# Performance work log

Measured on AMD Instinct MI355X. Metric: run time of the kernel, lower is better.

Reference implementation:

```python
import jax, jax.numpy as jnp
import numpy as np

PRIME_DELAYS = (1, 2, 3, 5)
LOCAL_LR = 0.05  # base_local_lr after clamp to [0, 0.99]


def _apply_delays(x, delay_gains):
    """OCNS phasal delay embedding. x: [B,T,D,2], delay_gains: [n_delays,D,2]."""
    x_eff = x
    for idx, tau in enumerate(PRIME_DELAYS):
        gr = delay_gains[idx, :, 0]
        gi = delay_gains[idx, :, 1]
        dr = x[:, :-tau, :, 0]
        di = x[:, :-tau, :, 1]
        upd = jnp.stack([dr * gr - di * gi, dr * gi + di * gr], axis=-1)
        x_eff = x_eff.at[:, tau:].add(upd)
    return x_eff


def _moe_expert_choice(xf, gate_bias, W_router, W1, W2, capacity):
    """Expert-choice MoE: each expert picks its top-`capacity` tokens.
    xf: [N,F] flattened complex features; returns [N,F]."""
    logits = xf @ W_router + gate_bias              # [N,E]
    scores = jax.nn.softmax(logits, axis=-1)        # [N,E]
    topv, topi = jax.lax.top_k(scores.T, capacity)  # each [E,C]
    xe = xf[topi]                                   # [E,C,F] gather
    h = jax.nn.gelu(jnp.einsum('ecf,efh->ech', xe, W1))
    ye = jnp.einsum('ech,ehf->ecf', h, W2) * topv[..., None]
    N, F = xf.shape
    return jnp.zeros((N, F), xf.dtype).at[topi.reshape(-1)].add(ye.reshape(-1, F))


def _forward(x_stream, delay_gains, Wg_spec, W_router, W1, W2, cos_p, sin_p, local_iters):
    x = jnp.nan_to_num(x_stream.astype(jnp.float32))
    B, T, D, _ = x.shape
    N = B * T
    E = W_router.shape[1]
    capacity = (2 * N) // E  # top-2-equivalent expert-choice token budget

    # spectral gate bias: per-token spectral magnitude -> expert logit bias [N,E]
    mag = jnp.sqrt(x[..., 0] ** 2 + x[..., 1] ** 2 + 1e-8)
    gate_bias = mag.reshape(N, D) @ Wg_spec

    # phase-rotated target: x_target[:, t] = rot(x[:, t-1]); x_target[:, 0] = x[:, 0]
    prev = x[:, :-1]
    rot_r = prev[..., 0] * cos_p - prev[..., 1] * sin_p
    rot_i = prev[..., 0] * sin_p + prev[..., 1] * cos_p
    x_target = jnp.concatenate([x[:, :1], jnp.stack([rot_r, rot_i], axis=-1)], axis=1)

    def step(xc, _):
        x_eff = _apply_delays(xc, delay_gains)
        pred = _moe_expert_choice(x_eff.reshape(N, 2 * D), gate_bias, W_router, W1, W2, capacity)
        pred = pred.reshape(B, T, D, 2)
        upd = jnp.clip(LOCAL_LR * (x_target - pred), -10.0, 10.0)
        return xc + upd, None

    out, _ = jax.lax.scan(step, x, None, length=local_iters)
    return out


def setup_inputs() -> dict:
    key = jax.random.key(0)
    ks = jax.random.split(key, 8)
    B, T, D, E = 2, 2048, 256, 64
    F = 2 * D
    phase = jax.random.uniform(ks[0], (D,)) * 2.0 * np.pi
    return {
        'x_stream': jax.random.normal(ks[1], (B, T, D, 2), jnp.float32) * 0.5,
        'delay_gains': jax.random.normal(ks[2], (len(PRIME_DELAYS), D, 2), jnp.float32) * 0.02,
        'Wg_spec': jax.random.normal(ks[3], (D, E), jnp.float32) / np.sqrt(D),
        'W_router': jax.random.normal(ks[4], (F, E), jnp.float32) / np.sqrt(F),
        'W1': jax.random.normal(ks[5], (E, F, F), jnp.float32) / np.sqrt(F),
        'W2': jax.random.normal(ks[6], (E, F, F), jnp.float32) / np.sqrt(F),
        'cos_p': jnp.cos(phase),
        'sin_p': jnp.sin(phase),
        'local_iters': 8,
    }


def reference(x_stream, delay_gains, Wg_spec, W_router, W1, W2, cos_p, sin_p, local_iters):
    return _forward(x_stream, delay_gains, Wg_spec, W_router, W1, W2, cos_p, sin_p, local_iters)
```

## Files before the change

kernel.cpp:

```cpp
#include <hip/hip_runtime.h>
#include <hip/hip_bf16.h>

#define TB 2
#define TT 2048
#define TD 256
#define TE 64
#define TF 512
#define TN 4096
#define TCAP 128
#define NITER 8

typedef __attribute__((ext_vector_type(8))) short bf16x8;
typedef __attribute__((ext_vector_type(4))) float f32x4;

__device__ inline float sanitize(float v){
  if (v != v) return 0.0f;
  const float FMAX = 3.402823466e+38f;
  if (v >  FMAX) return  FMAX;
  if (v < -FMAX) return -FMAX;
  return v;
}

__device__ inline short f2bf(float f){
  union { __hip_bfloat16 h; short s; } u;
  u.h = __float2bfloat16(f);
  return u.s;
}

__device__ inline float gelu_tanh(float x){
  float x3 = x*x*x;
  return 0.5f*x*(1.0f + tanhf(0.7978845608028654f*(x + 0.044715f*x3)));
}

__device__ __forceinline__ void gload16(const void* g, void* l){
  __builtin_amdgcn_global_load_lds(
      (__attribute__((address_space(1))) void*)g,
      (__attribute__((address_space(3))) void*)l, 16, 0, 0);
}


__global__ void k_init(const float* __restrict__ xs, const float* __restrict__ cosp,
                       const float* __restrict__ sinp, float* __restrict__ xw,
                       float* __restrict__ xt){
  int idx = blockIdx.x*256 + threadIdx.x;
  if (idx >= TN*TD) return;
  int d = idx & (TD-1);
  int n = idx >> 8;
  int t = n & (TT-1);
  float xr = sanitize(xs[2*idx]), xi = sanitize(xs[2*idx+1]);
  xw[2*idx] = xr; xw[2*idx+1] = xi;
  float tr, ti;
  if (t == 0){ tr = xr; ti = xi; }
  else {
    float pr = sanitize(xs[2*(idx-TD)]), pi = sanitize(xs[2*(idx-TD)+1]);
    float c = cosp[d], s = sinp[d];
    tr = pr*c - pi*s;
    ti = pr*s + pi*c;
  }
  xt[2*idx] = tr; xt[2*idx+1] = ti;
}

__global__ __launch_bounds__(64) void k_gatebias(const float* __restrict__ xw,
                                                 const float* __restrict__ wg,
                                                 float* __restrict__ gb){
  __shared__ float mag[TD];
  int n = blockIdx.x, t = threadIdx.x;
  for (int d = t; d < TD; d += 64){
    float xr = xw[(size_t)n*TF + 2*d], xi = xw[(size_t)n*TF + 2*d + 1];
    mag[d] = sqrtf(xr*xr + xi*xi + 1e-8f);
  }
  __syncthreads();
  float acc = 0.f;
  for (int d = 0; d < TD; d++) acc += mag[d]*wg[d*TE + t];
  gb[(size_t)n*TE + t] = acc;
}

__global__ __launch_bounds__(256) void k_castw(const float* __restrict__ W, short* __restrict__ Wt){
  __shared__ float tile[64][68];
  int e = blockIdx.y;
  int kt = (blockIdx.x >> 3) * 64;
  int nt = (blockIdx.x & 7) * 64;
  int tid = threadIdx.x;
  {
    int row = tid >> 4;
    int c4 = (tid & 15) * 4;
    #pragma unroll
    for (int i = 0; i < 4; i++){
      int r = row + i*16;
      float4 v = *(const float4*)(W + ((size_t)e*TF + kt + r)*TF + nt + c4);
      *(float4*)&tile[r][c4] = v;
    }
  }
  __syncthreads();
  #pragma unroll
  for (int i = 0; i < 2; i++){
    int un = tid + i*256;
    int nrow = un >> 3;
    int k8 = (un & 7) * 8;
    bf16x8 o;
    #pragma unroll
    for (int j = 0; j < 8; j++) o[j] = f2bf(tile[k8+j][nrow]);
    *(bf16x8*)(Wt + ((size_t)e*TF + nt + nrow)*TF + kt + k8) = o;
  }
}


__global__ __launch_bounds__(256) void k_combine(
    const float* __restrict__ xOld, float* __restrict__ xNew,
    const float* __restrict__ xt, const float* __restrict__ ye,
    const int* __restrict__ cnt, const int* __restrict__ list)
{
  int tid = threadIdx.x;
  int tok = tid >> 5;
  int kq  = (tid & 31) * 16;
  int n   = blockIdx.x*8 + tok;
  size_t off = (size_t)n*TF + kq;
  float p[16];
  #pragma unroll
  for (int q = 0; q < 16; q++) p[q] = 0.f;
  int c = cnt[n];
  for (int j = 0; j < c; j++){
    const float4* s = (const float4*)(ye + (size_t)list[n*64 + j]*TF + kq);
    #pragma unroll
    for (int k4 = 0; k4 < 4; k4++){
      float4 v = s[k4];
      p[4*k4+0] += v.x; p[4*k4+1] += v.y; p[4*k4+2] += v.z; p[4*k4+3] += v.w;
    }
  }
  const float4* a4 = (const float4*)(xOld + off);
  const float4* t4 = (const float4*)(xt + off);
  float4* o4 = (float4*)(xNew + off);
  #pragma unroll
  for (int j = 0; j < 4; j++){
    float4 a = a4[j], t = t4[j], o;
    float u;
    u = 0.05f*(t.x - p[4*j+0]); u = fminf(10.f, fmaxf(-10.f, u)); o.x = a.x + u;
    u = 0.05f*(t.y - p[4*j+1]); u = fminf(10.f, fmaxf(-10.f, u)); o.y = a.y + u;
    u = 0.05f*(t.z - p[4*j+2]); u = fminf(10.f, fmaxf(-10.f, u)); o.z = a.z + u;
    u = 0.05f*(t.w - p[4*j+3]); u = fminf(10.f, fmaxf(-10.f, u)); o.w = a.w + u;
    o4[j] = o;
  }
}


__global__ __launch_bounds__(256) void k_fuse2(
    const float* __restrict__ xcur, const float* __restrict__ g,
    const float* __restrict__ wr, const float* __restrict__ gb,
    short* __restrict__ xbf, float* __restrict__ scoresT)
{
  __shared__ float xeff[8][516];
  __shared__ float Bt[64][68];
  int tid = threadIdx.x;
  int tok = tid >> 5;
  int lane5 = tid & 31;
  int kq  = lane5 * 16;
  int n   = blockIdx.x*8 + tok;
  int t   = n & (TT-1);
  size_t rowoff = (size_t)n*TF + kq;

  float eff[16];
  {
    const float4* a4 = (const float4*)(xcur + rowoff);
    #pragma unroll
    for (int j = 0; j < 4; j++){
      float4 v = a4[j];
      eff[4*j+0] = v.x; eff[4*j+1] = v.y; eff[4*j+2] = v.z; eff[4*j+3] = v.w;
    }
  }
  const int taus[4] = {1,2,3,5};
  int d0 = kq >> 1;
  #pragma unroll
  for (int i = 0; i < 4; i++){
    int tau = taus[i];
    if (t >= tau){
      const float4* b4 = (const float4*)(xcur + rowoff - (size_t)tau*TF);
      float nb[16];
      #pragma unroll
      for (int j = 0; j < 4; j++){
        float4 v = b4[j];
        nb[4*j+0] = v.x; nb[4*j+1] = v.y; nb[4*j+2] = v.z; nb[4*j+3] = v.w;
      }
      #pragma unroll
      for (int p = 0; p < 8; p++){
        float gr = g[2*(i*TD + d0 + p)];
        float gi = g[2*(i*TD + d0 + p) + 1];
        eff[2*p]   += nb[2*p]*gr - nb[2*p+1]*gi;
        eff[2*p+1] += nb[2*p]*gi + nb[2*p+1]*gr;
      }
    }
  }
  {
    bf16x8 o0, o1;
    #pragma unroll
    for (int q = 0; q < 8; q++){ o0[q] = f2bf(eff[q]); o1[q] = f2bf(eff[8+q]); }
    *(bf16x8*)(xbf + rowoff)     = o0;
    *(bf16x8*)(xbf + rowoff + 8) = o1;
    #pragma unroll
    for (int jj = 0; jj < 4; jj++){
      int j = (jj + lane5) & 3;
      *(float4*)&xeff[tok][kq + 4*j] =
        make_float4(eff[4*j], eff[4*j+1], eff[4*j+2], eff[4*j+3]);
    }
  }
  __syncthreads();

  int tx = lane5;
  float acc0 = gb[(size_t)n*TE + 2*tx];
  float acc1 = gb[(size_t)n*TE + 2*tx + 1];
  int rB = tid >> 2, c16 = (tid & 3)*16;
  for (int kk = 0; kk < TF; kk += 64){
    #pragma unroll
    for (int jj = 0; jj < 4; jj++)
      *(float4*)&Bt[rB][c16 + 4*jj] = *(const float4*)(wr + (size_t)(kk+rB)*TE + c16 + 4*jj);
    __syncthreads();
    #pragma unroll
    for (int k = 0; k < 64; k++){
      float a = xeff[tok][kk + k];
      float2 b = *(const float2*)&Bt[k][2*tx];
      acc0 += a*b.x; acc1 += a*b.y;
    }
    __syncthreads();
  }
  float m = fmaxf(acc0, acc1);
  #pragma unroll
  for (int off = 1; off < 32; off <<= 1) m = fmaxf(m, __shfl_xor(m, off));
  float e0 = expf(acc0 - m), e1 = expf(acc1 - m);
  float s = e0 + e1;
  #pragma unroll
  for (int off = 1; off < 32; off <<= 1) s += __shfl_xor(s, off);
  float inv = 1.0f / s;
  scoresT[(size_t)(2*tx)*TN + n]     = e0*inv;
  scoresT[(size_t)(2*tx+1)*TN + n]   = e1*inv;
}

__global__ __launch_bounds__(1024) void k_topk2(const float* __restrict__ scoresT,
                                                int* __restrict__ topi, float* __restrict__ topv,
                                                int* __restrict__ cnt){
  int e = blockIdx.x;
  const float* sc = scoresT + (size_t)e*TN;
  __shared__ unsigned int hist[4096];
  __shared__ unsigned int chunkSum[64];
  __shared__ unsigned int s_prefix;
  __shared__ int s_k, s_cnt, s_min;
  int tid = threadIdx.x;
  if (tid < 64) cnt[e*64 + tid] = 0;
  unsigned int u[4];
  #pragma unroll
  for (int i = 0; i < 4; i++) u[i] = __float_as_uint(sc[tid + i*1024]);
  if (tid == 0){ s_prefix = 0u; s_k = TCAP; }

  const int shifts[3]  = {20, 8, 0};
  const int nbins[3]   = {4096, 4096, 256};
  const unsigned int pmasks[3] = {0u, 0xFFF00000u, 0xFFFFFF00u};
  for (int r = 0; r < 3; r++){
    int shift = shifts[r], nb = nbins[r];
    unsigned int bmask = (unsigned)nb - 1u;
    int logC = (nb == 4096) ? 6 : 2;
    for (int i = tid; i < nb; i += 1024) hist[i] = 0u;
    if (tid < 64) chunkSum[tid] = 0u;
    __syncthreads();
    unsigned int pref = s_prefix;
    unsigned int pmask = pmasks[r];
    #pragma unroll
    for (int i = 0; i < 4; i++)
      if ((u[i] & pmask) == pref) atomicAdd(&hist[(u[i] >> shift) & bmask], 1u);
    __syncthreads();
    for (int b = tid; b < nb; b += 1024){
      unsigned int h = hist[b];
      if (h) atomicAdd(&chunkSum[b >> logC], h);
    }
    __syncthreads();
    if (tid < 64){
      int chunk = 63 - tid;
      unsigned int s = chunkSum[chunk];
      unsigned int scan = s;
      #pragma unroll
      for (int d = 1; d < 64; d <<= 1){
        unsigned int t = __shfl_up(scan, d);
        if (tid >= d) scan += t;
      }
      unsigned int excl = scan - s;
      int k = s_k;
      if (excl < (unsigned)k && scan >= (unsigned)k){
        int C = 1 << logC;
        unsigned int cum = excl;
        for (int b = C-1; b >= 0; b--){
          unsigned int h = hist[(chunk << logC) + b];
          cum += h;
          if (cum >= (unsigned)k){
            s_k = k - (int)(cum - h);
            s_prefix = pref | ((unsigned)((chunk << logC) + b) << shift);
            break;
          }
        }
      }
    }
    __syncthreads();
  }
  unsigned int thr = s_prefix;
  int need_eq = s_k;
  if (tid == 0) s_cnt = 0;
  __syncthreads();
  #pragma unroll
  for (int i = 0; i < 4; i++){
    if (u[i] > thr){
      int p = atomicAdd(&s_cnt, 1);
      topi[e*TCAP + p] = tid + i*1024;
      topv[e*TCAP + p] = __uint_as_float(u[i]);
    }
  }
  __syncthreads();
  int base = s_cnt;
  int last = -1;
  for (int i = 0; i < need_eq; i++){
    __syncthreads();
    if (tid == 0) s_min = TN;
    __syncthreads();
    #pragma unroll
    for (int j = 0; j < 4; j++){
      int n = tid + j*1024;
      if (u[j] == thr && n > last) atomicMin(&s_min, n);
    }
    __syncthreads();
    int nsel = s_min;
    if (tid == 0){ topi[e*TCAP + base + i] = nsel; topv[e*TCAP + base + i] = __uint_as_float(thr); }
    last = nsel;
  }
}


__global__ __launch_bounds__(256) void k_gemm1c(const short* __restrict__ xbf,
                                                const short* __restrict__ W1t,
                                                const int* __restrict__ topi,
                                                short* __restrict__ hbf,
                                                int* __restrict__ cnt,
                                                int* __restrict__ list){
  __shared__ __align__(16) short As[2][128*64];
  __shared__ __align__(16) short Bs[2][64*64];
  __shared__ int rows[128];
  int bid = blockIdx.x;
  int swz = (bid & 7)*64 + (bid >> 3);
  int e = swz >> 3, n0 = (swz & 7)*64;
  int tid = threadIdx.x;
  if (tid < 128) rows[tid] = topi[e*TCAP + tid];
  __syncthreads();
  if (n0 == 0 && tid < 128){
    int n = rows[tid];
    int slot = atomicAdd(&cnt[n], 1);
    list[n*64 + slot] = e*TCAP + tid;
  }
  int rsub = tid >> 3;
  int cs = ((tid & 7) ^ (rsub & 7))*8;
  const short* sA0 = xbf + (size_t)rows[rsub      ]*TF + cs;
  const short* sA1 = xbf + (size_t)rows[rsub +  32]*TF + cs;
  const short* sA2 = xbf + (size_t)rows[rsub +  64]*TF + cs;
  const short* sA3 = xbf + (size_t)rows[rsub +  96]*TF + cs;
  const short* sB0 = W1t + ((size_t)e*TF + n0 + rsub)*TF + cs;
  const short* sB1 = sB0 + (size_t)32*TF;

  int w = tid >> 6, l = tid & 63;
  int lr = l & 15, lh = l >> 4;
  int lx = lr & 7;
  int ar0 = (32*w + lr)*64;
  int ar1 = ar0 + 16*64;
  int p0 = (lh ^ lx)*8;
  int p1 = ((4 + lh) ^ lx)*8;

  f32x4 acc[2][4];
  #pragma unroll
  for (int m = 0; m < 2; m++)
    #pragma unroll
    for (int j = 0; j < 4; j++)
      #pragma unroll
      for (int r = 0; r < 4; r++) acc[m][j][r] = 0.f;

  gload16(sA0, &As[0][        tid*8]);
  gload16(sA1, &As[0][2048 +  tid*8]);
  gload16(sA2, &As[0][4096 +  tid*8]);
  gload16(sA3, &As[0][6144 +  tid*8]);
  gload16(sB0, &Bs[0][        tid*8]);
  gload16(sB1, &Bs[0][2048 +  tid*8]);

  int cur = 0;
  for (int t = 0; t < 8; t++){
    if (t < 7){
      int kk = (t+1)*64;
      gload16(sA0 + kk, &As[cur^1][        tid*8]);
      gload16(sA1 + kk, &As[cur^1][2048 +  tid*8]);
      gload16(sA2 + kk, &As[cur^1][4096 +  tid*8]);
      gload16(sA3 + kk, &As[cur^1][6144 +  tid*8]);
      gload16(sB0 + kk, &Bs[cur^1][        tid*8]);
      gload16(sB1 + kk, &Bs[cur^1][2048 +  tid*8]);
      asm volatile("s_waitcnt vmcnt(6)" ::: "memory");
    } else {
      asm volatile("s_waitcnt vmcnt(0)" ::: "memory");
    }
    __builtin_amdgcn_sched_barrier(0);
    __builtin_amdgcn_s_barrier();
    __builtin_amdgcn_sched_barrier(0);
    #pragma unroll
    for (int kk = 0; kk < 2; kk++){
      int pc = kk ? p1 : p0;
      bf16x8 a0 = *(const bf16x8*)&As[cur][ar0 + pc];
      bf16x8 a1 = *(const bf16x8*)&As[cur][ar1 + pc];
      #pragma unroll
      for (int j = 0; j < 4; j++){
        bf16x8 b = *(const bf16x8*)&Bs[cur][(16*j + lr)*64 + pc];
        acc[0][j] = __builtin_amdgcn_mfma_f32_16x16x32_bf16(a0, b, acc[0][j], 0, 0, 0);
        acc[1][j] = __builtin_amdgcn_mfma_f32_16x16x32_bf16(a1, b, acc[1][j], 0, 0, 0);
      }
    }
    __builtin_amdgcn_sched_barrier(0);
    __builtin_amdgcn_s_barrier();
    cur ^= 1;
  }
  short* hdst = hbf + (size_t)e*TCAP*TF;
  #pragma unroll
  for (int m = 0; m < 2; m++)
    #pragma unroll
    for (int j = 0; j < 4; j++)
      #pragma unroll
      for (int r = 0; r < 4; r++){
        int row = 32*w + 16*m + lh*4 + r;
        int col = n0 + 16*j + lr;
        hdst[(size_t)row*TF + col] = f2bf(gelu_tanh(acc[m][j][r]));
      }
}

__global__ __launch_bounds__(256) void k_gemm2c(const short* __restrict__ hbf,
                                                const short* __restrict__ W2t,
                                                const int* __restrict__ topi,
                                                const float* __restrict__ topv,
                                                float* __restrict__ ye){
  __shared__ __align__(16) short As[2][128*64];
  __shared__ __align__(16) short Bs[2][64*64];
  __shared__ float tv[128];
  int bid = blockIdx.x;
  int swz = (bid & 7)*64 + (bid >> 3);
  int e = swz >> 3, n0 = (swz & 7)*64;
  int tid = threadIdx.x;
  if (tid < 128) tv[tid] = topv[e*TCAP + tid];
  __syncthreads();
  int rsub = tid >> 3;
  int cs = ((tid & 7) ^ (rsub & 7))*8;
  const short* sA0 = hbf + ((size_t)e*TCAP + rsub)*TF + cs;
  const short* sA1 = sA0 + (size_t)32*TF;
  const short* sA2 = sA0 + (size_t)64*TF;
  const short* sA3 = sA0 + (size_t)96*TF;
  const short* sB0 = W2t + ((size_t)e*TF + n0 + rsub)*TF + cs;
  const short* sB1 = sB0 + (size_t)32*TF;

  int w = tid >> 6, l = tid & 63;
  int lr = l & 15, lh = l >> 4;
  int lx = lr & 7;
  int ar0 = (32*w + lr)*64;
  int ar1 = ar0 + 16*64;
  int p0 = (lh ^ lx)*8;
  int p1 = ((4 + lh) ^ lx)*8;

  f32x4 acc[2][4];
  #pragma unroll
  for (int m = 0; m < 2; m++)
    #pragma unroll
    for (int j = 0; j < 4; j++)
      #pragma unroll
      for (int r = 0; r < 4; r++) acc[m][j][r] = 0.f;

  gload16(sA0, &As[0][        tid*8]);
  gload16(sA1, &As[0][2048 +  tid*8]);
  gload16(sA2, &As[0][4096 +  tid*8]);
  gload16(sA3, &As[0][6144 +  tid*8]);
  gload16(sB0, &Bs[0][        tid*8]);
  gload16(sB1, &Bs[0][2048 +  tid*8]);

  int cur = 0;
  for (int t = 0; t < 8; t++){
    if (t < 7){
      int kk = (t+1)*64;
      gload16(sA0 + kk, &As[cur^1][        tid*8]);
      gload16(sA1 + kk, &As[cur^1][2048 +  tid*8]);
      gload16(sA2 + kk, &As[cur^1][4096 +  tid*8]);
      gload16(sA3 + kk, &As[cur^1][6144 +  tid*8]);
      gload16(sB0 + kk, &Bs[cur^1][        tid*8]);
      gload16(sB1 + kk, &Bs[cur^1][2048 +  tid*8]);
      asm volatile("s_waitcnt vmcnt(6)" ::: "memory");
    } else {
      asm volatile("s_waitcnt vmcnt(0)" ::: "memory");
    }
    __builtin_amdgcn_sched_barrier(0);
    __builtin_amdgcn_s_barrier();
    __builtin_amdgcn_sched_barrier(0);
    #pragma unroll
    for (int kk = 0; kk < 2; kk++){
      int pc = kk ? p1 : p0;
      bf16x8 a0 = *(const bf16x8*)&As[cur][ar0 + pc];
      bf16x8 a1 = *(const bf16x8*)&As[cur][ar1 + pc];
      #pragma unroll
      for (int j = 0; j < 4; j++){
        bf16x8 b = *(const bf16x8*)&Bs[cur][(16*j + lr)*64 + pc];
        acc[0][j] = __builtin_amdgcn_mfma_f32_16x16x32_bf16(a0, b, acc[0][j], 0, 0, 0);
        acc[1][j] = __builtin_amdgcn_mfma_f32_16x16x32_bf16(a1, b, acc[1][j], 0, 0, 0);
      }
    }
    __builtin_amdgcn_sched_barrier(0);
    __builtin_amdgcn_s_barrier();
    cur ^= 1;
  }
  float* ydst = ye + (size_t)e*TCAP*TF;
  #pragma unroll
  for (int m = 0; m < 2; m++)
    #pragma unroll
    for (int j = 0; j < 4; j++)
      #pragma unroll
      for (int r = 0; r < 4; r++){
        int row = 32*w + 16*m + lh*4 + r;
        int col = n0 + 16*j + lr;
        ydst[(size_t)row*TF + col] = acc[m][j][r] * tv[row];
      }
}

extern "C" void kernel_launch(void* const* d_in, const int* in_sizes, int n_in,
                              void* d_out, int out_size, void* d_ws, size_t ws_size,
                              hipStream_t stream){
  (void)in_sizes; (void)n_in; (void)out_size; (void)ws_size;
  const float* x_stream = (const float*)d_in[0];
  const float* gains    = (const float*)d_in[1];
  const float* Wg       = (const float*)d_in[2];
  const float* Wr       = (const float*)d_in[3];
  const float* W1       = (const float*)d_in[4];
  const float* W2       = (const float*)d_in[5];
  const float* cosp     = (const float*)d_in[6];
  const float* sinp     = (const float*)d_in[7];

  size_t off = 0;
  char* base = (char*)d_ws;
  auto alloc = [&](size_t bytes) -> void* {
    void* p = base + off;
    off += (bytes + 255) & ~(size_t)255;
    return p;
  };
  float* X0      = (float*)alloc((size_t)TN*TF*4);
  float* X1      = (float*)alloc((size_t)TN*TF*4);
  float* x_targ  = (float*)alloc((size_t)TN*TF*4);
  short* xf_bf   = (short*)alloc((size_t)TN*TF*2);
  float* gateb   = (float*)alloc((size_t)TN*TE*4);
  float* scoresT = (float*)alloc((size_t)TE*TN*4);
  int*   topi    = (int*)  alloc((size_t)TE*TCAP*4);
  float* topv    = (float*)alloc((size_t)TE*TCAP*4);
  short* h_bf    = (short*)alloc((size_t)TE*TCAP*TF*2);
  float* ye      = (float*)alloc((size_t)TE*TCAP*TF*4);
  int*   cnt     = (int*)  alloc((size_t)TN*4);
  int*   list    = (int*)  alloc((size_t)TN*64*4);
  short* W1t     = (short*)alloc((size_t)TE*TF*TF*2);
  short* W2t     = (short*)alloc((size_t)TE*TF*TF*2);

  k_init<<<(TN*TD + 255)/256, 256, 0, stream>>>(x_stream, cosp, sinp, X0, x_targ);
  k_gatebias<<<TN, 64, 0, stream>>>(X0, Wg, gateb);
  k_castw<<<dim3(64, TE), 256, 0, stream>>>(W1, W1t);
  k_castw<<<dim3(64, TE), 256, 0, stream>>>(W2, W2t);

  float* cur = X0;
  float* nxt = X1;
  for (int it = 0; it < NITER; it++){
    if (it > 0){
      k_combine<<<TN/8, 256, 0, stream>>>(cur, nxt, x_targ, ye, cnt, list);
      float* tmp = cur; cur = nxt; nxt = tmp;
    }
    k_fuse2<<<TN/8, 256, 0, stream>>>(cur, gains, Wr, gateb, xf_bf, scoresT);
    k_topk2<<<TE, 1024, 0, stream>>>(scoresT, topi, topv, cnt);
    k_gemm1c<<<TF/64*TE, 256, 0, stream>>>(xf_bf, W1t, topi, h_bf, cnt, list);
    k_gemm2c<<<TF/64*TE, 256, 0, stream>>>(h_bf, W2t, topi, topv, ye);
  }
  k_combine<<<TN/8, 256, 0, stream>>>(cur, (float*)d_out, x_targ, ye, cnt, list);
}
```

Before: 628.9 us.

## Fuse combine into delay/router kernel and store expert outputs as bf16

```diff
diff --git a/kernel.cpp b/kernel.cpp
--- a/kernel.cpp
+++ b/kernel.cpp
@@ -25,6 +25,12 @@
   union { __hip_bfloat16 h; short s; } u;
   u.h = __float2bfloat16(f);
   return u.s;
+}
+
+__device__ inline float bf2f(short s){
+  union { float f; unsigned int u; } v;
+  v.u = ((unsigned int)(unsigned short)s) << 16;
+  return v.f;
 }
 
 __device__ inline float gelu_tanh(float x){
@@ -104,103 +110,109 @@
   }
 }
 
-
-__global__ __launch_bounds__(256) void k_combine(
+__device__ __forceinline__ void combine4(const float* __restrict__ xOld,
+                                         const float* __restrict__ xt,
+                                         const short* __restrict__ ye,
+                                         int c, const int* __restrict__ lst,
+                                         int nrow, int col, int upd, float* o){
+  size_t off = (size_t)nrow*TF + col;
+  float4 a = *(const float4*)(xOld + off);
+  if (upd){
+    float p0=0.f, p1=0.f, p2=0.f, p3=0.f;
+    for (int j = 0; j < c; j++){
+      short4 v = *(const short4*)(ye + (size_t)lst[j]*TF + col);
+      p0 += bf2f(v.x); p1 += bf2f(v.y); p2 += bf2f(v.z); p3 += bf2f(v.w);
+    }
+    float4 t = *(const float4*)(xt + off);
+    float u;
+    u = 0.05f*(t.x - p0); u = fminf(10.f, fmaxf(-10.f, u)); o[0] = a.x + u;
+    u = 0.05f*(t.y - p1); u = fminf(10.f, fmaxf(-10.f, u)); o[1] = a.y + u;
+    u = 0.05f*(t.z - p2); u = fminf(10.f, fmaxf(-10.f, u)); o[2] = a.z + u;
+    u = 0.05f*(t.w - p3); u = fminf(10.f, fmaxf(-10.f, u)); o[3] = a.w + u;
+  } else {
+    o[0] = a.x; o[1] = a.y; o[2] = a.z; o[3] = a.w;
+  }
+}
+
+
+__global__ __launch_bounds__(256) void k_step(
     const float* __restrict__ xOld, float* __restrict__ xNew,
-    const float* __restrict__ xt, const float* __restrict__ ye,
-    const int* __restrict__ cnt, const int* __restrict__ list)
+    const float* __restrict__ xt, const short* __restrict__ ye,
+    const int* __restrict__ cnt, const int* __restrict__ list,
+    const float* __restrict__ g, const float* __restrict__ wr,
+    const float* __restrict__ gb, short* __restrict__ xbf,
+    float* __restrict__ scoresT, int upd)
 {
-  int tid = threadIdx.x;
-  int tok = tid >> 5;
-  int kq  = (tid & 31) * 16;
-  int n   = blockIdx.x*8 + tok;
-  size_t off = (size_t)n*TF + kq;
-  float p[16];
-  #pragma unroll
-  for (int q = 0; q < 16; q++) p[q] = 0.f;
-  int c = cnt[n];
-  for (int j = 0; j < c; j++){
-    const float4* s = (const float4*)(ye + (size_t)list[n*64 + j]*TF + kq);
-    #pragma unroll
-    for (int k4 = 0; k4 < 4; k4++){
-      float4 v = s[k4];
-      p[4*k4+0] += v.x; p[4*k4+1] += v.y; p[4*k4+2] += v.z; p[4*k4+3] += v.w;
-    }
-  }
-  const float4* a4 = (const float4*)(xOld + off);
-  const float4* t4 = (const float4*)(xt + off);
-  float4* o4 = (float4*)(xNew + off);
-  #pragma unroll
-  for (int j = 0; j < 4; j++){
-    float4 a = a4[j], t = t4[j], o;
-    float u;
-    u = 0.05f*(t.x - p[4*j+0]); u = fminf(10.f, fmaxf(-10.f, u)); o.x = a.x + u;
-    u = 0.05f*(t.y - p[4*j+1]); u = fminf(10.f, fmaxf(-10.f, u)); o.y = a.y + u;
-    u = 0.05f*(t.z - p[4*j+2]); u = fminf(10.f, fmaxf(-10.f, u)); o.z = a.z + u;
-    u = 0.05f*(t.w - p[4*j+3]); u = fminf(10.f, fmaxf(-10.f, u)); o.w = a.w + u;
-    o4[j] = o;
-  }
-}
-
-
-__global__ __launch_bounds__(256) void k_fuse2(
-    const float* __restrict__ xcur, const float* __restrict__ g,
-    const float* __restrict__ wr, const float* __restrict__ gb,
-    short* __restrict__ xbf, float* __restrict__ scoresT)
-{
-  __shared__ float xeff[8][516];
+  __shared__ float xtile[13][516];
   __shared__ float Bt[64][68];
   int tid = threadIdx.x;
-  int tok = tid >> 5;
-  int lane5 = tid & 31;
-  int kq  = lane5 * 16;
-  int n   = blockIdx.x*8 + tok;
-  int t   = n & (TT-1);
-  size_t rowoff = (size_t)n*TF + kq;
+  int tok = tid >> 5, lane5 = tid & 31;
+  int nbase = blockIdx.x*8, n = nbase + tok, t = n & (TT-1);
+
+  float cur[16];
+  {
+    int c = upd ? cnt[n] : 0;
+    const int* lst = list + n*64;
+    #pragma unroll
+    for (int s = 0; s < 4; s++){
+      int col = 4*lane5 + 128*s;
+      combine4(xOld, xt, ye, c, lst, n, col, upd, cur + 4*s);
+      *(float4*)(xNew + (size_t)n*TF + col) =
+          make_float4(cur[4*s], cur[4*s+1], cur[4*s+2], cur[4*s+3]);
+      *(float4*)&xtile[5+tok][col] =
+          make_float4(cur[4*s], cur[4*s+1], cur[4*s+2], cur[4*s+3]);
+    }
+  }
+  if (tok < 5){
+    int hr = nbase - 5 + tok;
+    if (hr >= 0){
+      int c = upd ? cnt[hr] : 0;
+      const int* lst = list + hr*64;
+      #pragma unroll
+      for (int s = 0; s < 4; s++){
+        int col = 4*lane5 + 128*s;
+        float h[4];
+        combine4(xOld, xt, ye, c, lst, hr, col, upd, h);
+        *(float4*)&xtile[tok][col] = make_float4(h[0], h[1], h[2], h[3]);
+      }
+    }
+  }
+  __syncthreads();
 
   float eff[16];
-  {
-    const float4* a4 = (const float4*)(xcur + rowoff);
-    #pragma unroll
-    for (int j = 0; j < 4; j++){
-      float4 v = a4[j];
-      eff[4*j+0] = v.x; eff[4*j+1] = v.y; eff[4*j+2] = v.z; eff[4*j+3] = v.w;
-    }
-  }
+  #pragma unroll
+  for (int q = 0; q < 16; q++) eff[q] = cur[q];
   const int taus[4] = {1,2,3,5};
-  int d0 = kq >> 1;
   #pragma unroll
   for (int i = 0; i < 4; i++){
     int tau = taus[i];
     if (t >= tau){
-      const float4* b4 = (const float4*)(xcur + rowoff - (size_t)tau*TF);
-      float nb[16];
-      #pragma unroll
-      for (int j = 0; j < 4; j++){
-        float4 v = b4[j];
-        nb[4*j+0] = v.x; nb[4*j+1] = v.y; nb[4*j+2] = v.z; nb[4*j+3] = v.w;
-      }
-      #pragma unroll
-      for (int p = 0; p < 8; p++){
-        float gr = g[2*(i*TD + d0 + p)];
-        float gi = g[2*(i*TD + d0 + p) + 1];
-        eff[2*p]   += nb[2*p]*gr - nb[2*p+1]*gi;
-        eff[2*p+1] += nb[2*p]*gi + nb[2*p+1]*gr;
-      }
-    }
-  }
-  {
-    bf16x8 o0, o1;
-    #pragma unroll
-    for (int q = 0; q < 8; q++){ o0[q] = f2bf(eff[q]); o1[q] = f2bf(eff[8+q]); }
-    *(bf16x8*)(xbf + rowoff)     = o0;
-    *(bf16x8*)(xbf + rowoff + 8) = o1;
-    #pragma unroll
-    for (int jj = 0; jj < 4; jj++){
-      int j = (jj + lane5) & 3;
-      *(float4*)&xeff[tok][kq + 4*j] =
-        make_float4(eff[4*j], eff[4*j+1], eff[4*j+2], eff[4*j+3]);
-    }
+      int rrow = 5 + tok - tau;
+      #pragma unroll
+      for (int s = 0; s < 4; s++){
+        int col = 4*lane5 + 128*s;
+        float4 v = *(const float4*)&xtile[rrow][col];
+        int d = col >> 1;
+        float gr0 = g[2*(i*TD + d)],     gi0 = g[2*(i*TD + d) + 1];
+        float gr1 = g[2*(i*TD + d + 1)], gi1 = g[2*(i*TD + d + 1) + 1];
+        eff[4*s+0] += v.x*gr0 - v.y*gi0;
+        eff[4*s+1] += v.x*gi0 + v.y*gr0;
+        eff[4*s+2] += v.z*gr1 - v.w*gi1;
+        eff[4*s+3] += v.z*gi1 + v.w*gr1;
+      }
+    }
+  }
+  __syncthreads();
+
+  #pragma unroll
+  for (int s = 0; s < 4; s++){
+    int col = 4*lane5 + 128*s;
+    short4 ob;
+    ob.x = f2bf(eff[4*s+0]); ob.y = f2bf(eff[4*s+1]);
+    ob.z = f2bf(eff[4*s+2]); ob.w = f2bf(eff[4*s+3]);
+    *(short4*)(xbf + (size_t)n*TF + col) = ob;
+    *(float4*)&xtile[5+tok][col] =
+        make_float4(eff[4*s], eff[4*s+1], eff[4*s+2], eff[4*s+3]);
   }
   __syncthreads();
 
@@ -215,7 +227,7 @@
     __syncthreads();
     #pragma unroll
     for (int k = 0; k < 64; k++){
-      float a = xeff[tok][kk + k];
+      float a = xtile[5+tok][kk + k];
       float2 b = *(const float2*)&Bt[k][2*tx];
       acc0 += a*b.x; acc1 += a*b.y;
     }
@@ -231,6 +243,26 @@
   float inv = 1.0f / s;
   scoresT[(size_t)(2*tx)*TN + n]     = e0*inv;
   scoresT[(size_t)(2*tx+1)*TN + n]   = e1*inv;
+}
+
+__global__ __launch_bounds__(256) void k_combine(
+    const float* __restrict__ xOld, float* __restrict__ xNew,
+    const float* __restrict__ xt, const short* __restrict__ ye,
+    const int* __restrict__ cnt, const int* __restrict__ list)
+{
+  int tid = threadIdx.x;
+  int tok = tid >> 5;
+  int lane5 = tid & 31;
+  int n = blockIdx.x*8 + tok;
+  int c = cnt[n];
+  const int* lst = list + n*64;
+  #pragma unroll
+  for (int s = 0; s < 4; s++){
+    int col = 4*lane5 + 128*s;
+    float o[4];
+    combine4(xOld, xt, ye, c, lst, n, col, 1, o);
+    *(float4*)(xNew + (size_t)n*TF + col) = make_float4(o[0], o[1], o[2], o[3]);
+  }
 }
 
 __global__ __launch_bounds__(1024) void k_topk2(const float* __restrict__ scoresT,
@@ -431,7 +463,7 @@
                                                 const short* __restrict__ W2t,
                                                 const int* __restrict__ topi,
                                                 const float* __restrict__ topv,
-                                                float* __restrict__ ye){
+                                                short* __restrict__ ye){
   __shared__ __align__(16) short As[2][128*64];
   __shared__ __align__(16) short Bs[2][64*64];
   __shared__ float tv[128];
@@ -506,7 +538,7 @@
     __builtin_amdgcn_s_barrier();
     cur ^= 1;
   }
-  float* ydst = ye + (size_t)e*TCAP*TF;
+  short* ydst = ye + (size_t)e*TCAP*TF;
   #pragma unroll
   for (int m = 0; m < 2; m++)
     #pragma unroll
@@ -515,7 +547,7 @@
       for (int r = 0; r < 4; r++){
         int row = 32*w + 16*m + lh*4 + r;
         int col = n0 + 16*j + lr;
-        ydst[(size_t)row*TF + col] = acc[m][j][r] * tv[row];
+        ydst[(size_t)row*TF + col] = f2bf(acc[m][j][r] * tv[row]);
       }
 }
 
@@ -548,7 +580,7 @@
   int*   topi    = (int*)  alloc((size_t)TE*TCAP*4);
   float* topv    = (float*)alloc((size_t)TE*TCAP*4);
   short* h_bf    = (short*)alloc((size_t)TE*TCAP*TF*2);
-  float* ye      = (float*)alloc((size_t)TE*TCAP*TF*4);
+  short* ye      = (short*)alloc((size_t)TE*TCAP*TF*2);
   int*   cnt     = (int*)  alloc((size_t)TN*4);
   int*   list    = (int*)  alloc((size_t)TN*64*4);
   short* W1t     = (short*)alloc((size_t)TE*TF*TF*2);
@@ -562,11 +594,9 @@
   float* cur = X0;
   float* nxt = X1;
   for (int it = 0; it < NITER; it++){
-    if (it > 0){
-      k_combine<<<TN/8, 256, 0, stream>>>(cur, nxt, x_targ, ye, cnt, list);
-      float* tmp = cur; cur = nxt; nxt = tmp;
-    }
-    k_fuse2<<<TN/8, 256, 0, stream>>>(cur, gains, Wr, gateb, xf_bf, scoresT);
+    k_step<<<TN/8, 256, 0, stream>>>(cur, nxt, x_targ, ye, cnt, list, gains, Wr, gateb,
+                                     xf_bf, scoresT, it > 0 ? 1 : 0);
+    { float* tmp = cur; cur = nxt; nxt = tmp; }
     k_topk2<<<TE, 1024, 0, stream>>>(scoresT, topi, topv, cnt);
     k_gemm1c<<<TF/64*TE, 256, 0, stream>>>(xf_bf, W1t, topi, h_bf, cnt, list);
     k_gemm2c<<<TF/64*TE, 256, 0, stream>>>(h_bf, W2t, topi, topv, ye);
```

New measurement: 684.0 us. 1.09x slower.
